# Kernel tuning notes

Hardware: AMD Instinct MI355X
Metric: run time of the kernel (lower is better)

Reference implementation:

```python
import jax, jax.numpy as jnp
import numpy as np

STEPS = 32
LO, HI = 0.0, 1.0
BETA = 0.1
IMPULSE = float(1.0 / (abs(BETA) * np.sqrt(np.pi)))  # unused in fwd, kept for parity


def _cells(x):
    """Filtration values of all cells of the V-construction cubical complex.
    Vertices = pixels; edges = max of the 2 endpoint pixels; squares = max of 4 corners."""
    v = x                                                    # [B,C,H,W]   sign +1
    he = jnp.maximum(x[..., :, :-1], x[..., :, 1:])          # [B,C,H,W-1] sign -1
    ve = jnp.maximum(x[..., :-1, :], x[..., 1:, :])          # [B,C,H-1,W] sign -1
    sq = jnp.maximum(jnp.maximum(x[..., :-1, :-1], x[..., :-1, 1:]),
                     jnp.maximum(x[..., 1:, :-1], x[..., 1:, 1:]))  # [B,C,H-1,W-1] sign +1
    return v, he, ve, sq


def _ecc_forward(x):
    """Euler characteristic curve ECC(t) = #V(t) - #E(t) + #F(t) sampled on
    tseq = linspace(LO, HI, STEPS). Returns [B, C*STEPS] (flattened, matching nn.Flatten)."""
    B, C, H, W = x.shape
    BC = B * C
    tseq = jnp.linspace(LO, HI, STEPS, dtype=x.dtype)
    v, he, ve, sq = _cells(x)
    f = jnp.concatenate([v.reshape(BC, -1), he.reshape(BC, -1),
                         ve.reshape(BC, -1), sq.reshape(BC, -1)], axis=1)  # [BC, Ncells]
    signs = jnp.concatenate([
        jnp.ones(H * W, jnp.float32),
        -jnp.ones(H * (W - 1), jnp.float32),
        -jnp.ones((H - 1) * W, jnp.float32),
        jnp.ones((H - 1) * (W - 1), jnp.float32),
    ])
    # first threshold index j with tseq[j] >= f (cell is "alive" for all t >= idx)
    idx = jnp.searchsorted(tseq, f, side='left')            # [BC, Ncells], values in [0, STEPS]
    rows = jnp.arange(BC)[:, None]
    hist = jnp.zeros((BC, STEPS + 1), jnp.float32).at[rows, idx].add(signs[None, :])
    ecc = jnp.cumsum(hist[:, :STEPS], axis=1)               # [BC, STEPS]
    return ecc.reshape(B, C * STEPS)


def setup_inputs() -> dict:
    key = jax.random.key(0)
    x = jax.random.uniform(key, (64, 3, 224, 224), dtype=jnp.float32)
    return {"x": x}


def reference(x):
    return _ecc_forward(x)
```

## Files before the change

### kernel.cpp

```cpp
#include <hip/hip_runtime.h>
#include <hip/hip_bf16.h>


#define H 224
#define W 224
#define STEPS 32
#define NBINS 34
#define NCOL 64
#define BANDS 8
#define BAND_ROWS 28
#define SUB_ROWS 7
#define NTHR 256

__device__ __forceinline__ int bin_of(float f) {
    int i = (int)ceilf(f * 31.0f);
    return i > 31 ? 31 : i;
}

__global__ __launch_bounds__(NTHR, 4) void ecc_hist_kernel(
        const float* __restrict__ x, int* __restrict__ ghist)
{
    __shared__ int lh[NBINS * NCOL];
    __shared__ int partial[NTHR];

    const int tid = threadIdx.x;
    #pragma unroll
    for (int i = tid; i < NBINS * NCOL; i += NTHR) lh[i] = 0;
    __syncthreads();

    const int band = blockIdx.x & (BANDS - 1);
    const int img  = blockIdx.x / BANDS;
    const float* __restrict__ p = x + (size_t)img * (H * W);

    const int c = tid & 63;
    const int s = tid >> 6;

    if (c < 56) {
        const int  j0    = c << 2;
        const bool lastc = (c == 55);
        const int  jn    = lastc ? (W - 1) : (j0 + 4);
        const int  r0    = band * BAND_ROWS + s * SUB_ROWS;
        int* __restrict__ lhc = lh + c;

        float4 F = *(const float4*)(p + r0 * W + j0);
        float  fn = p[r0 * W + jn];
        int B0 = bin_of(F.x), B1 = bin_of(F.y), B2 = bin_of(F.z), B3 = bin_of(F.w);
        int Bn = lastc ? 33 : bin_of(fn);

        for (int r = r0; r < r0 + SUB_ROWS; ++r) {
            int C0, C1, C2, C3, Cn;
            if (r < H - 1) {
                float4 G = *(const float4*)(p + (r + 1) * W + j0);
                float  gn = p[(r + 1) * W + jn];
                C0 = bin_of(G.x); C1 = bin_of(G.y); C2 = bin_of(G.z); C3 = bin_of(G.w);
                Cn = lastc ? 33 : bin_of(gn);
            } else {
                C0 = C1 = C2 = C3 = 32; Cn = 32;
            }

            if (B1 > B0) { atomicAdd(&lhc[B0 << 6],  1); atomicAdd(&lhc[B1 << 6], -1); }
            if (B2 > B1) { atomicAdd(&lhc[B1 << 6],  1); atomicAdd(&lhc[B2 << 6], -1); }
            if (B3 > B2) { atomicAdd(&lhc[B2 << 6],  1); atomicAdd(&lhc[B3 << 6], -1); }
            if (Bn > B3) { atomicAdd(&lhc[B3 << 6],  1); atomicAdd(&lhc[Bn << 6], -1); }

            {
                int M0 = max(B0, C0), M1 = max(B1, C1), M2 = max(B2, C2),
                    M3 = max(B3, C3), Mn = max(Bn, Cn);
                if (M1 > M0) { atomicAdd(&lhc[M0 << 6], -1); atomicAdd(&lhc[M1 << 6], 1); }
                if (M2 > M1) { atomicAdd(&lhc[M1 << 6], -1); atomicAdd(&lhc[M2 << 6], 1); }
                if (M3 > M2) { atomicAdd(&lhc[M2 << 6], -1); atomicAdd(&lhc[M3 << 6], 1); }
                if (Mn > M3) { atomicAdd(&lhc[M3 << 6], -1); atomicAdd(&lhc[Mn << 6], 1); }
            }

            B0 = C0; B1 = C1; B2 = C2; B3 = C3; Bn = Cn;
        }
    }
    __syncthreads();

    const int b = tid >> 3;
    const int g = tid & 7;
    const int4* row = (const int4*)(lh + (b << 6) + (g << 3));
    int4 v0 = row[0], v1 = row[1];
    partial[tid] = v0.x + v0.y + v0.z + v0.w + v1.x + v1.y + v1.z + v1.w;
    __syncthreads();

    if (tid < 32) {
        const int4* pr = (const int4*)(partial + (tid << 3));
        int4 a0 = pr[0], a1 = pr[1];
        int s8 = a0.x + a0.y + a0.z + a0.w + a1.x + a1.y + a1.z + a1.w;
        atomicAdd(&ghist[img * STEPS + tid], s8);
    }
}

__global__ void ecc_cumsum_kernel(const int* __restrict__ ghist,
                                  float* __restrict__ out, int nimg)
{
    int img = blockIdx.x * blockDim.x + threadIdx.x;
    if (img < nimg) {
        int s = 0;
        #pragma unroll
        for (int t = 0; t < STEPS; ++t) {
            s += ghist[img * STEPS + t];
            out[img * STEPS + t] = (float)s;
        }
    }
}

extern "C" void kernel_launch(void* const* d_in, const int* in_sizes, int n_in,
                              void* d_out, int out_size, void* d_ws, size_t ws_size,
                              hipStream_t stream) {
    const float* x = (const float*)d_in[0];
    float* out = (float*)d_out;
    int* ghist = (int*)d_ws;

    const int nimg = in_sizes[0] / (H * W);

    hipMemsetAsync(ghist, 0, (size_t)nimg * STEPS * sizeof(int), stream);

    dim3 grid1(nimg * BANDS);
    ecc_hist_kernel<<<grid1, NTHR, 0, stream>>>(x, ghist);

    int thr2 = 256;
    int blk2 = (nimg + thr2 - 1) / thr2;
    ecc_cumsum_kernel<<<blk2, thr2, 0, stream>>>(ghist, out, nimg);
}
```

Measured before the change: 80.72 us.

## Replace global atomics and memset with per-band partials reduced in scan kernel

Each histogram block now writes its per-band 32-bin partial to a distinct workspace slot instead of atomically adding into a zeroed global histogram, which removes the memset launch and the global atomics. The cumsum kernel now uses one block per image: it sums the 8 band partials and does a wavefront shuffle prefix scan instead of a serial per-thread loop. Launch bounds are raised to 6 waves-per-SIMD hint for occupancy, and the last column's neighbor index is changed (value ignored since lastc forces bin 33). The workspace now needs 8x more space.

```diff
diff --git a/kernel.cpp b/kernel.cpp
--- a/kernel.cpp
+++ b/kernel.cpp
@@ -17,8 +17,8 @@
     return i > 31 ? 31 : i;
 }
 
-__global__ __launch_bounds__(NTHR, 4) void ecc_hist_kernel(
-        const float* __restrict__ x, int* __restrict__ ghist)
+__global__ __launch_bounds__(NTHR, 6) void ecc_hist_kernel(
+        const float* __restrict__ x, int* __restrict__ part)
 {
     __shared__ int lh[NBINS * NCOL];
     __shared__ int partial[NTHR];
@@ -38,7 +38,7 @@
     if (c < 56) {
         const int  j0    = c << 2;
         const bool lastc = (c == 55);
-        const int  jn    = lastc ? (W - 1) : (j0 + 4);
+        const int  jn    = lastc ? (j0 + 3) : (j0 + 4);
         const int  r0    = band * BAND_ROWS + s * SUB_ROWS;
         int* __restrict__ lhc = lh + c;
 
@@ -88,21 +88,26 @@
         const int4* pr = (const int4*)(partial + (tid << 3));
         int4 a0 = pr[0], a1 = pr[1];
         int s8 = a0.x + a0.y + a0.z + a0.w + a1.x + a1.y + a1.z + a1.w;
-        atomicAdd(&ghist[img * STEPS + tid], s8);
+        part[(((img << 3) | band) << 5) + tid] = s8;
     }
 }
 
-__global__ void ecc_cumsum_kernel(const int* __restrict__ ghist,
-                                  float* __restrict__ out, int nimg)
+__global__ __launch_bounds__(64) void ecc_cumsum_kernel(
+        const int* __restrict__ part, float* __restrict__ out)
 {
-    int img = blockIdx.x * blockDim.x + threadIdx.x;
-    if (img < nimg) {
+    const int img  = blockIdx.x;
+    const int lane = threadIdx.x;
+    if (lane < STEPS) {
+        const int* pb = part + (img << 8) + lane;
         int s = 0;
         #pragma unroll
-        for (int t = 0; t < STEPS; ++t) {
-            s += ghist[img * STEPS + t];
-            out[img * STEPS + t] = (float)s;
+        for (int band = 0; band < BANDS; ++band) s += pb[band << 5];
+        #pragma unroll
+        for (int off = 1; off < STEPS; off <<= 1) {
+            int v = __shfl_up(s, off);
+            if (lane >= off) s += v;
         }
+        out[img * STEPS + lane] = (float)s;
     }
 }
 
@@ -111,16 +116,12 @@
                               hipStream_t stream) {
     const float* x = (const float*)d_in[0];
     float* out = (float*)d_out;
-    int* ghist = (int*)d_ws;
+    int* part = (int*)d_ws;
 
     const int nimg = in_sizes[0] / (H * W);
 
-    hipMemsetAsync(ghist, 0, (size_t)nimg * STEPS * sizeof(int), stream);
+    dim3 grid1(nimg * BANDS);
+    ecc_hist_kernel<<<grid1, NTHR, 0, stream>>>(x, part);
 
-    dim3 grid1(nimg * BANDS);
-    ecc_hist_kernel<<<grid1, NTHR, 0, stream>>>(x, ghist);
-
-    int thr2 = 256;
-    int blk2 = (nimg + thr2 - 1) / thr2;
-    ecc_cumsum_kernel<<<blk2, thr2, 0, stream>>>(ghist, out, nimg);
+    ecc_cumsum_kernel<<<dim3(nimg), 64, 0, stream>>>(part, out);
 }
```

Result: no change. 79.15 us (-1.9%).
